# Kernel optimization log

Hardware: AMD Instinct MI355X
Metric: run time of the kernel (lower is better)

The kernel has to match this reference:

```python
import jax, jax.numpy as jnp
import numpy as np

D = 1024
H = 16
DH = D // H  # 64
FF_H = 4096
EPS = 1e-5


def layernorm(x, gamma, beta):
    mu = jnp.mean(x, axis=-1, keepdims=True)
    var = jnp.var(x, axis=-1, keepdims=True)
    return (x - mu) * jax.lax.rsqrt(var + EPS) * gamma + beta


def setup_inputs() -> dict:
    key = jax.random.key(0)
    ks = jax.random.split(key, 12)
    B, S = 2, 2048
    q = jax.random.normal(ks[0], (B, S, D), dtype=jnp.float32)
    k = jax.random.normal(ks[1], (B, S, D), dtype=jnp.float32)
    v = jax.random.normal(ks[2], (B, S, D), dtype=jnp.float32)
    time_lengths = jax.random.randint(ks[3], (B,), 0, S)
    mask = jnp.zeros((1, 1, S, S), dtype=jnp.float32)
    sc = 0.02
    Wq = jax.random.normal(ks[4], (D, D), dtype=jnp.float32) * sc
    Wk = jax.random.normal(ks[5], (D, D), dtype=jnp.float32) * sc
    Wv = jax.random.normal(ks[6], (D, D), dtype=jnp.float32) * sc
    Wd = jax.random.normal(ks[7], (D, D), dtype=jnp.float32) * sc
    W1 = jax.random.normal(ks[8], (D, FF_H), dtype=jnp.float32) * sc
    b1 = jnp.zeros((FF_H,), dtype=jnp.float32)
    W2 = jax.random.normal(ks[9], (FF_H, D), dtype=jnp.float32) * sc
    b2 = jnp.zeros((D,), dtype=jnp.float32)
    g1 = jnp.ones((D,), dtype=jnp.float32)
    be1 = jnp.zeros((D,), dtype=jnp.float32)
    g2 = jnp.ones((D,), dtype=jnp.float32)
    be2 = jnp.zeros((D,), dtype=jnp.float32)
    return {"q": q, "k": k, "v": v, "time_lengths": time_lengths, "mask": mask,
            "Wq": Wq, "Wk": Wk, "Wv": Wv, "Wd": Wd,
            "W1": W1, "b1": b1, "W2": W2, "b2": b2,
            "g1": g1, "be1": be1, "g2": g2, "be2": be2}


def reference(q, k, v, time_lengths, mask, Wq, Wk, Wv, Wd, W1, b1, W2, b2, g1, be1, g2, be2):
    B, S, _ = q.shape
    scale = jnp.sqrt(jnp.float32(DH))
    # project and split heads: [B,H,S,DH]
    qh = (q @ Wq).reshape(B, S, H, DH).transpose(0, 2, 1, 3)
    kh = (k @ Wk).reshape(B, S, H, DH).transpose(0, 2, 1, 3)
    vh = (v @ Wv).reshape(B, S, H, DH).transpose(0, 2, 1, 3)
    score = jnp.einsum('bhqd,bhkd->bhqk', qh, kh) / scale + mask
    attn = jax.nn.softmax(score, axis=-1)
    z = jnp.einsum('bhqk,bhkd->bhqd', attn, vh)
    z = z.transpose(0, 2, 1, 3).reshape(B, S, D)
    z = z @ Wd
    # Add & LayerNorm 1 (note: original applies LN to attn out, then adds q)
    x = layernorm(z, g1, be1) + q
    # FF (dropout is identity in eval)
    ff = jax.nn.relu(x @ W1 + b1) @ W2 + b2
    return layernorm(ff + x, g2, be2)
```

## Files before the change

kernel.cpp:

```cpp
#include <hip/hip_runtime.h>
#include <hip/hip_bf16.h>


#define SEQ 2048
#define DM  1024
#define LNEPS 1e-5f

typedef __attribute__((ext_vector_type(8))) short bf16x8;
typedef __attribute__((ext_vector_type(4))) float f32x4;

#define GAS __attribute__((address_space(1)))
#define LAS __attribute__((address_space(3)))

static __device__ __forceinline__ void gl_lds16(const unsigned short* g, unsigned short* l) {
    __builtin_amdgcn_global_load_lds((const GAS void*)g, (LAS void*)l, 16, 0, 0);
}

static __device__ __forceinline__ unsigned short f2bf(float f) {
    unsigned u = __builtin_bit_cast(unsigned, f);
    u += 0x7fffu + ((u >> 16) & 1u);
    return (unsigned short)(u >> 16);
}

static __device__ __forceinline__ unsigned cvt_pk_bf16(float lo, float hi) {
    unsigned r;
    asm("v_cvt_pk_bf16_f32 %0, %1, %2" : "=v"(r) : "v"(lo), "v"(hi));
    return r;
}

__global__ __launch_bounds__(512) void gemm256(
    const unsigned short* __restrict__ A, const unsigned short* __restrict__ Bt,
    unsigned short* __restrict__ Cb,
    int N, int Klen, int lda, int ldb,
    const float* __restrict__ bias, int lgn)
{
    __shared__ unsigned short Asl[2][2][128 * 64];
    __shared__ unsigned short Bsl[2][2][128 * 64];

    const int t = threadIdx.x, lane = t & 63, w = t >> 6;
    const int wm = w >> 2, wn = w & 3;
    const int l15 = lane & 15, l16 = lane >> 4;

    const int nwg = gridDim.x;
    const int sw = (blockIdx.x & 7) * (nwg >> 3) + (blockIdx.x >> 3);
    const int n0 = (sw & ((1 << lgn) - 1)) * 256;
    const int m0 = (sw >> lgn) * 256;

    const int sr = t >> 3, sc = t & 7;
    const int gcs = (sc ^ (sr & 7)) * 8;

    f32x4 acc[8][4];
    #pragma unroll
    for (int i = 0; i < 8; i++)
        #pragma unroll
        for (int j = 0; j < 4; j++)
            acc[i][j] = (f32x4){0.f, 0.f, 0.f, 0.f};

    auto STAGEPAIR = [&](int kt, int ph) {
        const int slot = kt & 1;
        if (ph < 2) {
            #pragma unroll
            for (int p = 0; p < 2; p++)
                gl_lds16(&A[(size_t)(m0 + ph * 128 + p * 64 + sr) * lda + kt * 64 + gcs],
                         &Asl[slot][ph][p * 4096 + w * 512]);
        } else {
            const int h = ph - 2;
            #pragma unroll
            for (int p = 0; p < 2; p++)
                gl_lds16(&Bt[(size_t)(n0 + h * 128 + p * 64 + sr) * ldb + kt * 64 + gcs],
                         &Bsl[slot][h][p * 4096 + w * 512]);
        }
    };

    #pragma unroll
    for (int ph = 0; ph < 4; ph++) STAGEPAIR(0, ph);

    const int NT = Klen >> 6;
    for (int T = 0; T < NT; T++) {
        const int slot = T & 1;
        const int Tn = (T + 1 < NT) ? T + 1 : 0;

        bf16x8 afr[4][2], bfr[2][2];

        auto LOADA = [&](int MH) {
            #pragma unroll
            for (int mi = 0; mi < 4; mi++)
                #pragma unroll
                for (int kk = 0; kk < 2; kk++) {
                    const int r = MH * 64 + mi * 16 + l15;
                    afr[mi][kk] = *(const bf16x8*)
                        &Asl[slot][wm][r * 64 + (((kk * 4 + l16) ^ (r & 7)) * 8)];
                }
        };
        auto LOADB = [&](int NH) {
            #pragma unroll
            for (int ni = 0; ni < 2; ni++)
                #pragma unroll
                for (int kk = 0; kk < 2; kk++) {
                    const int r = (wn & 1) * 64 + NH * 32 + ni * 16 + l15;
                    bfr[ni][kk] = *(const bf16x8*)
                        &Bsl[slot][wn >> 1][r * 64 + (((kk * 4 + l16) ^ (r & 7)) * 8)];
                }
        };
        auto MFMA16 = [&](int MH, int NH) {
            __builtin_amdgcn_s_setprio(1);
            #pragma unroll
            for (int mi = 0; mi < 4; mi++)
                #pragma unroll
                for (int ni = 0; ni < 2; ni++) {
                    acc[MH * 4 + mi][NH * 2 + ni] = __builtin_amdgcn_mfma_f32_16x16x32_bf16(
                        afr[mi][0], bfr[ni][0], acc[MH * 4 + mi][NH * 2 + ni], 0, 0, 0);
                    acc[MH * 4 + mi][NH * 2 + ni] = __builtin_amdgcn_mfma_f32_16x16x32_bf16(
                        afr[mi][1], bfr[ni][1], acc[MH * 4 + mi][NH * 2 + ni], 0, 0, 0);
                }
            __builtin_amdgcn_s_setprio(0);
        };

        STAGEPAIR(Tn, 0);
        asm volatile("s_waitcnt vmcnt(2)" ::: "memory");
        __builtin_amdgcn_s_barrier();
        __builtin_amdgcn_sched_barrier(0);
        LOADA(0); LOADB(0);
        asm volatile("s_waitcnt lgkmcnt(0)" ::: "memory");
        __builtin_amdgcn_sched_barrier(0);
        MFMA16(0, 0);
        __builtin_amdgcn_s_barrier();

        STAGEPAIR(Tn, 1);
        __builtin_amdgcn_s_barrier();
        __builtin_amdgcn_sched_barrier(0);
        LOADB(1);
        asm volatile("s_waitcnt lgkmcnt(0)" ::: "memory");
        __builtin_amdgcn_sched_barrier(0);
        MFMA16(0, 1);
        __builtin_amdgcn_s_barrier();

        STAGEPAIR(Tn, 2);
        __builtin_amdgcn_s_barrier();
        __builtin_amdgcn_sched_barrier(0);
        LOADA(1);
        asm volatile("s_waitcnt lgkmcnt(0)" ::: "memory");
        __builtin_amdgcn_sched_barrier(0);
        MFMA16(1, 1);
        __builtin_amdgcn_s_barrier();

        STAGEPAIR(Tn, 3);
        __builtin_amdgcn_s_barrier();
        __builtin_amdgcn_sched_barrier(0);
        LOADB(0);
        asm volatile("s_waitcnt lgkmcnt(0)" ::: "memory");
        __builtin_amdgcn_sched_barrier(0);
        MFMA16(1, 0);
        __builtin_amdgcn_s_barrier();
    }

    asm volatile("s_waitcnt vmcnt(0)" ::: "memory");

    #pragma unroll
    for (int f = 0; f < 8; f++) {
        const int row0 = m0 + wm * 128 + (f >> 2) * 64 + (f & 3) * 16 + l16 * 4;
        #pragma unroll
        for (int g = 0; g < 4; g++) {
            const int col = n0 + wn * 64 + (g >> 1) * 32 + (g & 1) * 16 + l15;
            const float bv = bias[col];
            #pragma unroll
            for (int r = 0; r < 4; r++) {
                float vv = fmaxf(acc[f][g][r] + bv, 0.f);
                Cb[(size_t)(row0 + r) * N + col] = f2bf(vv);
            }
        }
    }
}

__global__ __launch_bounds__(256) void gemm_bf16(
    const unsigned short* __restrict__ A, const unsigned short* __restrict__ Bt,
    float* __restrict__ Cf, unsigned short* __restrict__ Cb,
    unsigned short* __restrict__ CbT,
    int M, int N, int Klen, int lda, int ldb,
    size_t sA, size_t sB, size_t sC,
    const float* __restrict__ bias, int ep, int lgn)
{
    __shared__ unsigned short As[2][128 * 32];
    __shared__ unsigned short Bs[2][128 * 32];

    const int t = threadIdx.x, lane = t & 63, w = t >> 6;
    const int wm = w >> 1, wn = w & 1;

    const int nwg = gridDim.x;
    const int sw = (blockIdx.x & 7) * (nwg >> 3) + (blockIdx.x >> 3);
    const int n0 = (sw & ((1 << lgn) - 1)) * 128;
    const int m0 = (sw >> lgn) * 128;

    A  += (size_t)blockIdx.z * sA;
    Bt += (size_t)blockIdx.z * sB;
    const size_t cbase = (size_t)blockIdx.z * sC;
    const int l15 = lane & 15, l16 = lane >> 4;
    const int ar = lane >> 2, ac = (lane & 3) * 8;

    f32x4 acc[4][4];
    #pragma unroll
    for (int i = 0; i < 4; i++)
        #pragma unroll
        for (int j = 0; j < 4; j++)
            acc[i][j] = (f32x4){0.f, 0.f, 0.f, 0.f};

    auto stage = [&](int buf, int k0) {
        #pragma unroll
        for (int i = 0; i < 2; i++) {
            const int rg = w * 2 + i;
            gl_lds16(&A [(size_t)(m0 + rg * 16 + ar) * lda + k0 + ac], &As[buf][rg * 512]);
            gl_lds16(&Bt[(size_t)(n0 + rg * 16 + ar) * ldb + k0 + ac], &Bs[buf][rg * 512]);
        }
    };
    auto compute = [&](int buf) {
        bf16x8 af[4], bfr[4];
        #pragma unroll
        for (int i = 0; i < 4; i++) {
            af[i]  = *(const bf16x8*)&As[buf][(wm * 64 + i * 16 + l15) * 32 + l16 * 8];
            bfr[i] = *(const bf16x8*)&Bs[buf][(wn * 64 + i * 16 + l15) * 32 + l16 * 8];
        }
        #pragma unroll
        for (int mi = 0; mi < 4; mi++)
            #pragma unroll
            for (int ni = 0; ni < 4; ni++)
                acc[mi][ni] = __builtin_amdgcn_mfma_f32_16x16x32_bf16(
                    af[mi], bfr[ni], acc[mi][ni], 0, 0, 0);
    };

    stage(0, 0);
    __syncthreads();
    int k0 = 0;
    for (; k0 + 32 < Klen; k0 += 32) {
        const int cur = (k0 >> 5) & 1;
        stage(cur ^ 1, k0 + 32);
        compute(cur);
        __syncthreads();
    }
    compute((k0 >> 5) & 1);

    if (CbT && blockIdx.z == 2) {
        #pragma unroll
        for (int ni = 0; ni < 4; ni++) {
            const int col = n0 + wn * 64 + ni * 16 + l15;
            const int hh = col >> 6, d = col & 63;
            #pragma unroll
            for (int mi = 0; mi < 4; mi++) {
                const int row = m0 + wm * 64 + mi * 16 + l16 * 4;
                const int bb = row >> 11, s = row & 2047;
                ushort4 o;
                o.x = f2bf(acc[mi][ni][0]); o.y = f2bf(acc[mi][ni][1]);
                o.z = f2bf(acc[mi][ni][2]); o.w = f2bf(acc[mi][ni][3]);
                *(ushort4*)&CbT[((size_t)((bb * 16 + hh) * 64 + d)) * SEQ + s] = o;
            }
        }
        return;
    }

    #pragma unroll
    for (int ni = 0; ni < 4; ni++) {
        const int col = n0 + wn * 64 + ni * 16 + l15;
        const float bv = (ep && blockIdx.z == 0) ? bias[col] : 0.f;
        #pragma unroll
        for (int mi = 0; mi < 4; mi++) {
            #pragma unroll
            for (int r = 0; r < 4; r++) {
                const int row = m0 + wm * 64 + mi * 16 + l16 * 4 + r;
                float vv = acc[mi][ni][r] + bv;
                if (ep == 2) vv = fmaxf(vv, 0.f);
                if (Cf) Cf[cbase + (size_t)row * N + col] = vv;
                else    Cb[cbase + (size_t)row * N + col] = f2bf(vv);
            }
        }
    }
}

__global__ __launch_bounds__(256) void attn_mfma(
    const unsigned short* __restrict__ qh, const unsigned short* __restrict__ kh,
    const unsigned short* __restrict__ vhT, const float* __restrict__ mask,
    unsigned short* __restrict__ z)
{
    __shared__ unsigned short Ks0[64 * 64];
    __shared__ unsigned short Ks1[64 * 64];
    __shared__ unsigned short Vst[64 * 64];
    __shared__ unsigned short Ps[64 * 72];

    const int t = threadIdx.x, lane = t & 63, w = t >> 6;
    const int bid = blockIdx.x;
    const int qt = bid >> 5, h = bid & 15, b = (bid >> 4) & 1;
    const int q0 = qt * 64, qr = w * 16;
    const int l15 = lane & 15, l16 = lane >> 4;

    const int lr = lane >> 3;
    const int gc = ((lane & 7) ^ lr) * 8;

    const size_t qbase = (size_t)(b * SEQ + q0) * DM + h * 64;
    const size_t kbase = (size_t)(b * SEQ) * DM + h * 64;
    const size_t vbase = (size_t)((b * 16 + h) * 64) * SEQ;

    #pragma unroll
    for (int i = 0; i < 2; i++) {
        const int rg = w * 2 + i;
        gl_lds16(&qh[qbase + (size_t)(rg * 8 + lr) * DM + gc], &Ks1[rg * 512]);
        gl_lds16(&kh[kbase + (size_t)(rg * 8 + lr) * DM + gc], &Ks0[rg * 512]);
    }
    __syncthreads();

    const int sw0 = ((l16    ) ^ (l15 & 7)) * 8;
    const int sw1 = ((l16 + 4) ^ (l15 & 7)) * 8;
    const bf16x8 bQ0 = *(const bf16x8*)&Ks1[(qr + l15) * 64 + sw0];
    const bf16x8 bQ1 = *(const bf16x8*)&Ks1[(qr + l15) * 64 + sw1];
    __syncthreads();

    const float* mrow = mask + (size_t)(q0 + qr + l15) * SEQ;

    float m_i = -1e30f, l_i = 0.f;
    f32x4 o4[4];
    #pragma unroll
    for (int mi = 0; mi < 4; mi++) o4[mi] = (f32x4){0.f, 0.f, 0.f, 0.f};

    for (int kt = 0; kt < SEQ / 64; kt++) {
        const int k0 = kt * 64;
        const int kn = ((kt + 1) & (SEQ / 64 - 1)) * 64;
        unsigned short* Kcur = (kt & 1) ? Ks1 : Ks0;
        unsigned short* Knxt = (kt & 1) ? Ks0 : Ks1;

        __builtin_amdgcn_s_barrier();

        float4 mv[4];
        #pragma unroll
        for (int ki = 0; ki < 4; ki++)
            mv[ki] = *(const float4*)&mrow[k0 + ki * 16 + l16 * 4];

        #pragma unroll
        for (int i = 0; i < 2; i++) {
            const int rg = w * 2 + i;
            gl_lds16(&vhT[vbase + (size_t)(rg * 8 + lr) * SEQ + k0 + gc], &Vst[rg * 512]);
        }
        __builtin_amdgcn_sched_barrier(0);
        #pragma unroll
        for (int i = 0; i < 2; i++) {
            const int rg = w * 2 + i;
            gl_lds16(&kh[kbase + (size_t)(kn + rg * 8 + lr) * DM + gc], &Knxt[rg * 512]);
        }

        asm volatile("s_waitcnt vmcnt(8)" ::: "memory");
        __builtin_amdgcn_s_barrier();
        __builtin_amdgcn_sched_barrier(0);

        f32x4 s4[4];
        __builtin_amdgcn_s_setprio(1);
        #pragma unroll
        for (int ki = 0; ki < 4; ki++) {
            const int r = ki * 16 + l15;
            const bf16x8 aK0 = *(const bf16x8*)&Kcur[r * 64 + sw0];
            const bf16x8 aK1 = *(const bf16x8*)&Kcur[r * 64 + sw1];
            f32x4 a0 = (f32x4){0.f, 0.f, 0.f, 0.f};
            a0 = __builtin_amdgcn_mfma_f32_16x16x32_bf16(aK0, bQ0, a0, 0, 0, 0);
            s4[ki] = __builtin_amdgcn_mfma_f32_16x16x32_bf16(aK1, bQ1, a0, 0, 0, 0);
        }
        __builtin_amdgcn_s_setprio(0);

        float sv[16];
        #pragma unroll
        for (int ki = 0; ki < 4; ki++) {
            sv[ki * 4 + 0] = s4[ki][0] * 0.125f + mv[ki].x;
            sv[ki * 4 + 1] = s4[ki][1] * 0.125f + mv[ki].y;
            sv[ki * 4 + 2] = s4[ki][2] * 0.125f + mv[ki].z;
            sv[ki * 4 + 3] = s4[ki][3] * 0.125f + mv[ki].w;
        }

        float rm = fmaxf(sv[0], sv[1]);
        #pragma unroll
        for (int i = 2; i < 16; i += 2) rm = fmaxf(fmaxf(rm, sv[i]), sv[i + 1]);
        rm = fmaxf(rm, __shfl_xor(rm, 16));
        rm = fmaxf(rm, __shfl_xor(rm, 32));

        const bool skip = __all(rm <= m_i + 8.f);
        float mnew = m_i, alpha = 1.f;
        if (!skip) { mnew = fmaxf(m_i, rm); alpha = __expf(m_i - mnew); }

        float ps = 0.f;
        #pragma unroll
        for (int ki = 0; ki < 4; ki++) {
            const float p0 = __expf(sv[ki * 4 + 0] - mnew);
            const float p1 = __expf(sv[ki * 4 + 1] - mnew);
            const float p2 = __expf(sv[ki * 4 + 2] - mnew);
            const float p3 = __expf(sv[ki * 4 + 3] - mnew);
            ps += (p0 + p1) + (p2 + p3);
            uint2 pk;
            pk.x = cvt_pk_bf16(p0, p1);
            pk.y = cvt_pk_bf16(p2, p3);
            *(uint2*)&Ps[(qr + l15) * 72 + ki * 16 + l16 * 4] = pk;
        }
        ps += __shfl_xor(ps, 16);
        ps += __shfl_xor(ps, 32);
        if (!skip) {
            m_i = mnew;
            l_i = l_i * alpha + ps;
            #pragma unroll
            for (int mi = 0; mi < 4; mi++)
                #pragma unroll
                for (int r = 0; r < 4; r++) o4[mi][r] *= alpha;
        } else {
            l_i += ps;
        }

        asm volatile("s_waitcnt vmcnt(2)" ::: "memory");
        __builtin_amdgcn_s_barrier();
        __builtin_amdgcn_sched_barrier(0);

        const bf16x8 bP0 = *(const bf16x8*)&Ps[(qr + l15) * 72 + l16 * 8];
        const bf16x8 bP1 = *(const bf16x8*)&Ps[(qr + l15) * 72 + 32 + l16 * 8];
        __builtin_amdgcn_s_setprio(1);
        #pragma unroll
        for (int mi = 0; mi < 4; mi++) {
            const int r = mi * 16 + l15;
            const bf16x8 aV0 = *(const bf16x8*)&Vst[r * 64 + sw0];
            const bf16x8 aV1 = *(const bf16x8*)&Vst[r * 64 + sw1];
            o4[mi] = __builtin_amdgcn_mfma_f32_16x16x32_bf16(aV0, bP0, o4[mi], 0, 0, 0);
            o4[mi] = __builtin_amdgcn_mfma_f32_16x16x32_bf16(aV1, bP1, o4[mi], 0, 0, 0);
        }
        __builtin_amdgcn_s_setprio(0);
    }

    asm volatile("s_waitcnt vmcnt(0)" ::: "memory");

    const float inv = 1.f / l_i;
    #pragma unroll
    for (int mi = 0; mi < 4; mi++) {
        const float a0 = o4[mi][0] * inv, a1 = o4[mi][1] * inv;
        const float a2 = o4[mi][2] * inv, a3 = o4[mi][3] * inv;
        uint2 ov;
        ov.x = cvt_pk_bf16(a0, a1);
        ov.y = cvt_pk_bf16(a2, a3);
        *(uint2*)&z[(size_t)(b * SEQ + q0 + qr + l15) * DM + h * 64 + mi * 16 + l16 * 4] = ov;
    }
}

__global__ __launch_bounds__(256) void prep(
    const float* __restrict__ q, const float* __restrict__ k, const float* __restrict__ v,
    unsigned short* __restrict__ qb,
    const float* __restrict__ Wq, const float* __restrict__ Wk,
    const float* __restrict__ Wv, const float* __restrict__ Wd,
    const float* __restrict__ W1, const float* __restrict__ W2,
    unsigned short* __restrict__ Wqt, unsigned short* __restrict__ Wdt,
    unsigned short* __restrict__ W1t, unsigned short* __restrict__ W2t)
{
    const int z = blockIdx.z, t = threadIdx.x;
    const int flat = blockIdx.y * 64 + blockIdx.x;

    if (z < 3) {
        const float* src = z == 0 ? q : (z == 1 ? k : v);
        unsigned short* dst = qb + (size_t)z * ((size_t)SEQ * 2 * DM);
        const size_t base = (size_t)flat * 4096 + t * 4;
        #pragma unroll
        for (int i = 0; i < 4; i++) {
            const float4 w4 = *(const float4*)&src[base + i * 1024];
            ushort4 o; o.x = f2bf(w4.x); o.y = f2bf(w4.y); o.z = f2bf(w4.z); o.w = f2bf(w4.w);
            *(ushort4*)&dst[base + i * 1024] = o;
        }
        return;
    }

    __shared__ float ts[64][65];
    const float* W; unsigned short* Wt; int K, N, n0, k0;
    if (z < 7) {
        if (flat >= 256) return;
        W  = z == 3 ? Wq : z == 4 ? Wk : (z == 5 ? Wv : Wd);
        Wt = z == 3 ? Wqt : z == 4 ? Wqt + 1024 * 1024
           : z == 5 ? Wqt + 2 * 1024 * 1024 : Wdt;
        K = 1024; N = 1024;
        n0 = (flat & 15) * 64; k0 = (flat >> 4) * 64;
    } else if (z == 7) {
        W = W1; Wt = W1t; K = 1024; N = 4096;
        n0 = blockIdx.x * 64; k0 = blockIdx.y * 64;
    } else {
        W = W2; Wt = W2t; K = 4096; N = 1024;
        n0 = (flat & 15) * 64; k0 = (flat >> 4) * 64;
    }

    const int r = t >> 4, c4 = (t & 15) * 4;
    #pragma unroll
    for (int i = 0; i < 4; i++) {
        const float4 v4 = *(const float4*)&W[(size_t)(k0 + r + i * 16) * N + n0 + c4];
        ts[r + i * 16][c4 + 0] = v4.x; ts[r + i * 16][c4 + 1] = v4.y;
        ts[r + i * 16][c4 + 2] = v4.z; ts[r + i * 16][c4 + 3] = v4.w;
    }
    __syncthreads();
    #pragma unroll
    for (int i = 0; i < 4; i++) {
        const int n = r + i * 16;
        ushort4 o;
        o.x = f2bf(ts[c4 + 0][n]); o.y = f2bf(ts[c4 + 1][n]);
        o.z = f2bf(ts[c4 + 2][n]); o.w = f2bf(ts[c4 + 3][n]);
        *(ushort4*)&Wt[(size_t)(n0 + n) * K + k0 + c4] = o;
    }
}

__global__ __launch_bounds__(256) void ln_res(
    const float* __restrict__ a, const float* __restrict__ a2,
    const float* __restrict__ a3, const float* __restrict__ a4,
    const float* __restrict__ r,
    const float* __restrict__ g, const float* __restrict__ be,
    float* __restrict__ out, unsigned short* __restrict__ outb, int mode)
{
    __shared__ float redls[8];
    const int row = blockIdx.x, t = threadIdx.x;
    const size_t base = (size_t)row * DM;

    float vals[4], s = 0.f, sq = 0.f;
    #pragma unroll
    for (int i = 0; i < 4; i++) {
        const int c = t + 256 * i;
        float x = a[base + c];
        if (a2) x += a2[base + c];
        if (a3) x += a3[base + c];
        if (a4) x += a4[base + c];
        if (mode == 1) x += r[base + c];
        vals[i] = x; s += x; sq += x * x;
    }
    #pragma unroll
    for (int off = 32; off > 0; off >>= 1) { s += __shfl_down(s, off); sq += __shfl_down(sq, off); }
    if ((t & 63) == 0) { redls[t >> 6] = s; redls[4 + (t >> 6)] = sq; }
    __syncthreads();
    s  = redls[0] + redls[1] + redls[2] + redls[3];
    sq = redls[4] + redls[5] + redls[6] + redls[7];

    const float mu  = s * (1.f / 1024.f);
    const float var = sq * (1.f / 1024.f) - mu * mu;
    const float rs  = rsqrtf(var + LNEPS);
    #pragma unroll
    for (int i = 0; i < 4; i++) {
        const int c = t + 256 * i;
        float y = (vals[i] - mu) * rs * g[c] + be[c];
        if (mode == 0) y += r[base + c];
        out[base + c] = y;
        if (outb) outb[base + c] = f2bf(y);
    }
}

extern "C" void kernel_launch(void* const* d_in, const int* in_sizes, int n_in,
                              void* d_out, int out_size, void* d_ws, size_t ws_size,
                              hipStream_t stream)
{
    const float* q    = (const float*)d_in[0];
    const float* k    = (const float*)d_in[1];
    const float* v    = (const float*)d_in[2];
    const float* mask = (const float*)d_in[4];
    const float* Wq   = (const float*)d_in[5];
    const float* Wk   = (const float*)d_in[6];
    const float* Wv   = (const float*)d_in[7];
    const float* Wd   = (const float*)d_in[8];
    const float* W1   = (const float*)d_in[9];
    const float* b1   = (const float*)d_in[10];
    const float* W2   = (const float*)d_in[11];
    const float* b2   = (const float*)d_in[12];
    const float* g1   = (const float*)d_in[13];
    const float* be1  = (const float*)d_in[14];
    const float* g2   = (const float*)d_in[15];
    const float* be2  = (const float*)d_in[16];
    float* out = (float*)d_out;

    char* WS = (char*)d_ws;
    const size_t MiB = 1u << 20;
    const size_t ND  = (size_t)4096 * 1024;

    unsigned short* qb  = (unsigned short*)(WS + 0);
    unsigned short* zb  = (unsigned short*)(WS + 8 * MiB);
    unsigned short* xb  = (unsigned short*)(WS + 16 * MiB);
    unsigned short* Wqt = (unsigned short*)(WS + 24 * MiB);
    unsigned short* Wdt = (unsigned short*)(WS + 30 * MiB);
    unsigned short* W1t = (unsigned short*)(WS + 32 * MiB);
    unsigned short* W2t = (unsigned short*)(WS + 40 * MiB);
    unsigned short* qh  = (unsigned short*)(WS + 48 * MiB);
    unsigned short* vhT = (unsigned short*)(WS + 64 * MiB);
    float*          zd0 = (float*)(WS + 48 * MiB);
    float*          zd1 = (float*)(WS + 64 * MiB);
    float*          x   = (float*)(WS + 80 * MiB);
    unsigned short* h1  = (unsigned short*)(WS + 96 * MiB);
    float*          y0  = (float*)(WS + 48 * MiB);
    float*          y1  = (float*)(WS + 64 * MiB);

    unsigned short* kh = qh + ND;

    const dim3 blk(256);

    prep<<<dim3(64, 16, 9), blk, 0, stream>>>(q, k, v, qb, Wq, Wk, Wv, Wd, W1, W2,
                                              Wqt, Wdt, W1t, W2t);

    gemm_bf16<<<dim3(256, 1, 3), blk, 0, stream>>>(qb, Wqt, nullptr, qh, vhT,
        4096, 1024, 1024, 1024, 1024, ND, (size_t)1024 * 1024, ND, nullptr, 0, 3);

    attn_mfma<<<dim3(1024), blk, 0, stream>>>(qh, kh, vhT, mask, zb);

    gemm_bf16<<<dim3(256, 1, 2), blk, 0, stream>>>(zb, Wdt, zd0, nullptr, nullptr,
        4096, 1024, 512, 1024, 1024, 512, 512, ND, nullptr, 0, 3);

    ln_res<<<dim3(4096), blk, 0, stream>>>(zd0, zd1, nullptr, nullptr, q,
                                           g1, be1, x, xb, 0);

    gemm256<<<dim3(256), dim3(512), 0, stream>>>(xb, W1t, h1,
        4096, 1024, 1024, 1024, b1, 4);

    gemm_bf16<<<dim3(256, 1, 2), blk, 0, stream>>>(h1, W2t, y0, nullptr, nullptr,
        4096, 1024, 2048, 4096, 4096, 2048, 2048, ND, b2, 1, 3);

    ln_res<<<dim3(4096), blk, 0, stream>>>(y0, y1, nullptr, nullptr, x,
                                           g2, be2, out, nullptr, 1);
}
```

Baseline: 455.1 us.

## Use 256-tile GEMM for QKV projections and widen attention to 128-query blocks

The batched QKV projection moves from the 128x128 gemm_bf16 kernel to the 256x256 gemm256 kernel. gemm256 is generalised with batch strides, an optional bias/ReLU epilogue, and the transposed V output path. The attention kernel now runs 512 threads covering 128 queries per block, so each loaded K/V tile is reused across twice as many queries and the grid is halved. Each wave now issues fewer global-to-LDS loads, and the vmcnt waits are adjusted to match. Risks are lower occupancy from the larger blocks and a grid of only 192 blocks for the QKV GEMM.

Result: no change. 455.1 us (-0.0%).

```diff
diff --git a/kernel.cpp b/kernel.cpp
--- a/kernel.cpp
+++ b/kernel.cpp
@@ -30,9 +30,10 @@
 
 __global__ __launch_bounds__(512) void gemm256(
     const unsigned short* __restrict__ A, const unsigned short* __restrict__ Bt,
-    unsigned short* __restrict__ Cb,
+    unsigned short* __restrict__ Cb, unsigned short* __restrict__ CbT,
     int N, int Klen, int lda, int ldb,
-    const float* __restrict__ bias, int lgn)
+    size_t sA, size_t sB, size_t sC,
+    const float* __restrict__ bias, int ep, int lgn)
 {
     __shared__ unsigned short Asl[2][2][128 * 64];
     __shared__ unsigned short Bsl[2][2][128 * 64];
@@ -45,6 +46,10 @@
     const int sw = (blockIdx.x & 7) * (nwg >> 3) + (blockIdx.x >> 3);
     const int n0 = (sw & ((1 << lgn) - 1)) * 256;
     const int m0 = (sw >> lgn) * 256;
+
+    A  += (size_t)blockIdx.z * sA;
+    Bt += (size_t)blockIdx.z * sB;
+    const size_t cbase = (size_t)blockIdx.z * sC;
 
     const int sr = t >> 3, sc = t & 7;
     const int gcs = (sc ^ (sr & 7)) * 8;
@@ -156,17 +161,36 @@
 
     asm volatile("s_waitcnt vmcnt(0)" ::: "memory");
 
+    if (CbT && blockIdx.z == 2) {
+        #pragma unroll
+        for (int f = 0; f < 8; f++) {
+            const int row0 = m0 + wm * 128 + (f >> 2) * 64 + (f & 3) * 16 + l16 * 4;
+            const int bb = row0 >> 11, s = row0 & 2047;
+            #pragma unroll
+            for (int g = 0; g < 4; g++) {
+                const int col = n0 + wn * 64 + (g >> 1) * 32 + (g & 1) * 16 + l15;
+                const int hh = col >> 6, d = col & 63;
+                ushort4 o;
+                o.x = f2bf(acc[f][g][0]); o.y = f2bf(acc[f][g][1]);
+                o.z = f2bf(acc[f][g][2]); o.w = f2bf(acc[f][g][3]);
+                *(ushort4*)&CbT[((size_t)((bb * 16 + hh) * 64 + d)) * SEQ + s] = o;
+            }
+        }
+        return;
+    }
+
     #pragma unroll
     for (int f = 0; f < 8; f++) {
         const int row0 = m0 + wm * 128 + (f >> 2) * 64 + (f & 3) * 16 + l16 * 4;
         #pragma unroll
         for (int g = 0; g < 4; g++) {
             const int col = n0 + wn * 64 + (g >> 1) * 32 + (g & 1) * 16 + l15;
-            const float bv = bias[col];
+            const float bv = ep ? bias[col] : 0.f;
             #pragma unroll
             for (int r = 0; r < 4; r++) {
-                float vv = fmaxf(acc[f][g][r] + bv, 0.f);
-                Cb[(size_t)(row0 + r) * N + col] = f2bf(vv);
+                float vv = acc[f][g][r] + bv;
+                if (ep == 2) vv = fmaxf(vv, 0.f);
+                Cb[cbase + (size_t)(row0 + r) * N + col] = f2bf(vv);
             }
         }
     }
@@ -175,7 +199,6 @@
 __global__ __launch_bounds__(256) void gemm_bf16(
     const unsigned short* __restrict__ A, const unsigned short* __restrict__ Bt,
     float* __restrict__ Cf, unsigned short* __restrict__ Cb,
-    unsigned short* __restrict__ CbT,
     int M, int N, int Klen, int lda, int ldb,
     size_t sA, size_t sB, size_t sC,
     const float* __restrict__ bias, int ep, int lgn)
@@ -238,24 +261,6 @@
     }
     compute((k0 >> 5) & 1);
 
-    if (CbT && blockIdx.z == 2) {
-        #pragma unroll
-        for (int ni = 0; ni < 4; ni++) {
-            const int col = n0 + wn * 64 + ni * 16 + l15;
-            const int hh = col >> 6, d = col & 63;
-            #pragma unroll
-            for (int mi = 0; mi < 4; mi++) {
-                const int row = m0 + wm * 64 + mi * 16 + l16 * 4;
-                const int bb = row >> 11, s = row & 2047;
-                ushort4 o;
-                o.x = f2bf(acc[mi][ni][0]); o.y = f2bf(acc[mi][ni][1]);
-                o.z = f2bf(acc[mi][ni][2]); o.w = f2bf(acc[mi][ni][3]);
-                *(ushort4*)&CbT[((size_t)((bb * 16 + hh) * 64 + d)) * SEQ + s] = o;
-            }
-        }
-        return;
-    }
-
     #pragma unroll
     for (int ni = 0; ni < 4; ni++) {
         const int col = n0 + wn * 64 + ni * 16 + l15;
@@ -274,7 +279,7 @@
     }
 }
 
-__global__ __launch_bounds__(256) void attn_mfma(
+__global__ __launch_bounds__(512) void attn_mfma(
     const unsigned short* __restrict__ qh, const unsigned short* __restrict__ kh,
     const unsigned short* __restrict__ vhT, const float* __restrict__ mask,
     unsigned short* __restrict__ z)
@@ -282,12 +287,12 @@
     __shared__ unsigned short Ks0[64 * 64];
     __shared__ unsigned short Ks1[64 * 64];
     __shared__ unsigned short Vst[64 * 64];
-    __shared__ unsigned short Ps[64 * 72];
+    __shared__ unsigned short Ps[128 * 72];
 
     const int t = threadIdx.x, lane = t & 63, w = t >> 6;
     const int bid = blockIdx.x;
     const int qt = bid >> 5, h = bid & 15, b = (bid >> 4) & 1;
-    const int q0 = qt * 64, qr = w * 16;
+    const int q0 = qt * 128, qr = w * 16;
     const int l15 = lane & 15, l16 = lane >> 4;
 
     const int lr = lane >> 3;
@@ -300,15 +305,15 @@
     #pragma unroll
     for (int i = 0; i < 2; i++) {
         const int rg = w * 2 + i;
-        gl_lds16(&qh[qbase + (size_t)(rg * 8 + lr) * DM + gc], &Ks1[rg * 512]);
-        gl_lds16(&kh[kbase + (size_t)(rg * 8 + lr) * DM + gc], &Ks0[rg * 512]);
-    }
+        gl_lds16(&qh[qbase + (size_t)(rg * 8 + lr) * DM + gc], &Ps[rg * 512]);
+    }
+    gl_lds16(&kh[kbase + (size_t)(w * 8 + lr) * DM + gc], &Ks0[w * 512]);
     __syncthreads();
 
     const int sw0 = ((l16    ) ^ (l15 & 7)) * 8;
     const int sw1 = ((l16 + 4) ^ (l15 & 7)) * 8;
-    const bf16x8 bQ0 = *(const bf16x8*)&Ks1[(qr + l15) * 64 + sw0];
-    const bf16x8 bQ1 = *(const bf16x8*)&Ks1[(qr + l15) * 64 + sw1];
+    const bf16x8 bQ0 = *(const bf16x8*)&Ps[(qr + l15) * 64 + sw0];
+    const bf16x8 bQ1 = *(const bf16x8*)&Ps[(qr + l15) * 64 + sw1];
     __syncthreads();
 
     const float* mrow = mask + (size_t)(q0 + qr + l15) * SEQ;
@@ -331,19 +336,11 @@
         for (int ki = 0; ki < 4; ki++)
             mv[ki] = *(const float4*)&mrow[k0 + ki * 16 + l16 * 4];
 
-        #pragma unroll
-        for (int i = 0; i < 2; i++) {
-            const int rg = w * 2 + i;
-            gl_lds16(&vhT[vbase + (size_t)(rg * 8 + lr) * SEQ + k0 + gc], &Vst[rg * 512]);
-        }
-        __builtin_amdgcn_sched_barrier(0);
-        #pragma unroll
-        for (int i = 0; i < 2; i++) {
-            const int rg = w * 2 + i;
-            gl_lds16(&kh[kbase + (size_t)(kn + rg * 8 + lr) * DM + gc], &Knxt[rg * 512]);
-        }
-
-        asm volatile("s_waitcnt vmcnt(8)" ::: "memory");
+        gl_lds16(&vhT[vbase + (size_t)(w * 8 + lr) * SEQ + k0 + gc], &Vst[w * 512]);
+        __builtin_amdgcn_sched_barrier(0);
+        gl_lds16(&kh[kbase + (size_t)(kn + w * 8 + lr) * DM + gc], &Knxt[w * 512]);
+
+        asm volatile("s_waitcnt vmcnt(6)" ::: "memory");
         __builtin_amdgcn_s_barrier();
         __builtin_amdgcn_sched_barrier(0);
 
@@ -405,7 +402,7 @@
             l_i += ps;
         }
 
-        asm volatile("s_waitcnt vmcnt(2)" ::: "memory");
+        asm volatile("s_waitcnt vmcnt(1)" ::: "memory");
         __builtin_amdgcn_s_barrier();
         __builtin_amdgcn_sched_barrier(0);
 
@@ -588,21 +585,21 @@
     prep<<<dim3(64, 16, 9), blk, 0, stream>>>(q, k, v, qb, Wq, Wk, Wv, Wd, W1, W2,
                                               Wqt, Wdt, W1t, W2t);
 
-    gemm_bf16<<<dim3(256, 1, 3), blk, 0, stream>>>(qb, Wqt, nullptr, qh, vhT,
-        4096, 1024, 1024, 1024, 1024, ND, (size_t)1024 * 1024, ND, nullptr, 0, 3);
-
-    attn_mfma<<<dim3(1024), blk, 0, stream>>>(qh, kh, vhT, mask, zb);
-
-    gemm_bf16<<<dim3(256, 1, 2), blk, 0, stream>>>(zb, Wdt, zd0, nullptr, nullptr,
+    gemm256<<<dim3(64, 1, 3), dim3(512), 0, stream>>>(qb, Wqt, qh, vhT,
+        1024, 1024, 1024, 1024, ND, (size_t)1024 * 1024, ND, nullptr, 0, 2);
+
+    attn_mfma<<<dim3(512), dim3(512), 0, stream>>>(qh, kh, vhT, mask, zb);
+
+    gemm_bf16<<<dim3(256, 1, 2), blk, 0, stream>>>(zb, Wdt, zd0, nullptr,
         4096, 1024, 512, 1024, 1024, 512, 512, ND, nullptr, 0, 3);
 
     ln_res<<<dim3(4096), blk, 0, stream>>>(zd0, zd1, nullptr, nullptr, q,
                                            g1, be1, x, xb, 0);
 
-    gemm256<<<dim3(256), dim3(512), 0, stream>>>(xb, W1t, h1,
-        4096, 1024, 1024, 1024, b1, 4);
-
-    gemm_bf16<<<dim3(256, 1, 2), blk, 0, stream>>>(h1, W2t, y0, nullptr, nullptr,
+    gemm256<<<dim3(256, 1, 1), dim3(512), 0, stream>>>(xb, W1t, h1, nullptr,
+        4096, 1024, 1024, 1024, 0, 0, 0, b1, 2, 4);
+
+    gemm_bf16<<<dim3(256, 1, 2), blk, 0, stream>>>(h1, W2t, y0, nullptr,
         4096, 1024, 2048, 4096, 4096, 2048, 2048, ND, b2, 1, 3);
 
     ln_res<<<dim3(4096), blk, 0, stream>>>(y0, y1, nullptr, nullptr, x,
```
